# Kernel tuning notes

Hardware: AMD Instinct MI355X
Metric: run time of the kernel (lower is better)

The kernel has to match this reference:

```python
import jax, jax.numpy as jnp
import numpy as np

EPS = 1e-5
ROPE_BASE = 10000.0


def _layernorm(x, g, b):
    mu = jnp.mean(x, axis=-1, keepdims=True)
    var = jnp.mean(jnp.square(x - mu), axis=-1, keepdims=True)
    return (x - mu) * jax.lax.rsqrt(var + EPS) * g + b


def _rope(q, k):
    # q, k: (B, T, H, D); rotate interleaved pairs along last dim, positions over T
    T, D = q.shape[1], q.shape[-1]
    half = D // 2
    inv_freq = ROPE_BASE ** (-jnp.arange(half, dtype=jnp.float32) / half)
    ang = jnp.arange(T, dtype=jnp.float32)[:, None] * inv_freq  # (T, half)
    cos = jnp.cos(ang)[None, :, None, :]
    sin = jnp.sin(ang)[None, :, None, :]

    def rot(x):
        xr, xi = x[..., 0::2], x[..., 1::2]
        yr = xr * cos - xi * sin
        yi = xr * sin + xi * cos
        return jnp.stack([yr, yi], axis=-1).reshape(x.shape)

    return rot(q), rot(k)


def setup_inputs() -> dict:
    key = jax.random.key(0)
    ks = jax.random.split(key, 5)
    E, F, B, T = 1024, 4096, 2, 2048
    s = 0.02
    return {
        "x": jax.random.normal(ks[0], (B, T, E), jnp.float32),
        "in_proj_w": jax.random.normal(ks[1], (3 * E, E), jnp.float32) * s,
        "out_proj_w": jax.random.normal(ks[2], (E, E), jnp.float32) * s,
        "ln1_g": jnp.ones((E,), jnp.float32),
        "ln1_b": jnp.zeros((E,), jnp.float32),
        "ln2_g": jnp.ones((E,), jnp.float32),
        "ln2_b": jnp.zeros((E,), jnp.float32),
        "w1": jax.random.normal(ks[3], (F, E), jnp.float32) * s,
        "w2": jax.random.normal(ks[4], (E, F), jnp.float32) * s,
        "context": 256,
    }


def reference(x, in_proj_w, out_proj_w, ln1_g, ln1_b, ln2_g, ln2_b, w1, w2, context):
    B, T, E = x.shape
    H = 16
    D = E // H

    # ---- self-attention block (pre-norm, residual) ----
    h = _layernorm(x, ln1_g, ln1_b)
    proj = h @ in_proj_w.T  # (B, T, 3E)
    qkv = proj.reshape(B, T, 3, H, D)
    q = qkv[:, :, 0]  # (B, T, H, D)
    k = qkv[:, :, 1]
    v = qkv[:, :, 2].transpose(0, 2, 1, 3)  # (B, H, T, D)
    q, k = _rope(q, k)
    q = q.transpose(0, 2, 1, 3)  # (B, H, T, D)
    k = k.transpose(0, 2, 1, 3)

    pos = jnp.arange(T)
    delta = pos[:, None] - pos[None, :]  # (T, T)
    mask = (delta >= 0) & (delta < context)

    scores = jnp.einsum("bhtd,bhsd->bhts", q, k) / jnp.sqrt(jnp.float32(D))
    scores = jnp.where(mask[None, None], scores, jnp.float32(-1e30))
    attn = jax.nn.softmax(scores, axis=-1)
    o = jnp.einsum("bhts,bhsd->bhtd", attn, v)
    o = o.transpose(0, 2, 1, 3).reshape(B, T, E)
    x = x + o @ out_proj_w.T

    # ---- FFN block (pre-norm, residual) ----
    h = _layernorm(x, ln2_g, ln2_b)
    update = jax.nn.gelu(h @ w1.T, approximate=False) @ w2.T
    return x + update
```

## Files before the change

### kernel.cpp

```cpp
#include <hip/hip_runtime.h>
#include <math.h>

#define B_BATCH 2
#define T_SEQ   2048
#define E_DIM   1024
#define H_HEADS 16
#define D_HEAD  64
#define F_DIM   4096
#define M_ROWS  (B_BATCH * T_SEQ)

typedef __attribute__((ext_vector_type(8))) short short8;
typedef __attribute__((ext_vector_type(4))) float floatx4;
typedef __attribute__((ext_vector_type(8))) unsigned short ushortx8;

typedef __attribute__((address_space(1))) const void global_cvoid;
typedef __attribute__((address_space(3))) void lds_void;

__device__ __forceinline__ unsigned short f2bf(float f) {
    unsigned u = __float_as_uint(f);
    u += 0x7fffu + ((u >> 16) & 1u);
    return (unsigned short)(u >> 16);
}
__device__ __forceinline__ float bf2f(unsigned short h) {
    return __uint_as_float(((unsigned)h) << 16);
}

__device__ __forceinline__ unsigned lds_lo(const void* p) {
    return (unsigned)(unsigned long long)p;
}

__device__ __forceinline__ float gelu_f(float v) {
    const float x = fabsf(v) * 0.70710678118654752f;
    const float t = __builtin_amdgcn_rcpf(__builtin_fmaf(0.3275911f, x, 1.0f));
    float p = __builtin_fmaf(1.061405429f, t, -1.453152027f);
    p = __builtin_fmaf(p, t, 1.421413741f);
    p = __builtin_fmaf(p, t, -0.284496736f);
    p = __builtin_fmaf(p, t, 0.254829592f);
    p *= t;
    const float e = __expf(-x * x);
    float er = __builtin_fmaf(-p, e, 1.0f);
    er = copysignf(er, v);
    return 0.5f * v * (1.0f + er);
}

__device__ __forceinline__ float waveReduceSum(float v) {
#pragma unroll
    for (int off = 32; off > 0; off >>= 1) v += __shfl_xor(v, off, 64);
    return v;
}

__global__ __launch_bounds__(256) void cvt_kernel(const float* __restrict__ in,
                                                  unsigned short* __restrict__ out,
                                                  int n) {
    const int i = (blockIdx.x * 256 + threadIdx.x) * 4;
    if (i >= n) return;
    float4 v = *(const float4*)(in + i);
    ushort4 o;
    o.x = f2bf(v.x); o.y = f2bf(v.y); o.z = f2bf(v.z); o.w = f2bf(v.w);
    *(ushort4*)(out + i) = o;
}

__global__ __launch_bounds__(256) void reduce4_kernel(const float* __restrict__ p,
                                                      float* __restrict__ out, int n) {
    const int i = (blockIdx.x * 256 + threadIdx.x) * 4;
    if (i >= n) return;
    float4 a  = *(const float4*)(out + i);
    float4 b0 = *(const float4*)(p + i);
    float4 b1 = *(const float4*)(p + (size_t)n + i);
    float4 b2 = *(const float4*)(p + 2 * (size_t)n + i);
    float4 b3 = *(const float4*)(p + 3 * (size_t)n + i);
    a.x += b0.x + b1.x + b2.x + b3.x;
    a.y += b0.y + b1.y + b2.y + b3.y;
    a.z += b0.z + b1.z + b2.z + b3.z;
    a.w += b0.w + b1.w + b2.w + b3.w;
    *(float4*)(out + i) = a;
}

__global__ __launch_bounds__(256) void rope_tab_kernel(float* __restrict__ tab) {
    const int idx = blockIdx.x * 256 + threadIdx.x;
    const int pos = idx >> 5, i = idx & 31;
    const float invf = powf(10000.0f, -(float)i / 32.0f);
    const float ang = (float)pos * invf;
    tab[idx * 2]     = cosf(ang);
    tab[idx * 2 + 1] = sinf(ang);
}

__global__ __launch_bounds__(256) void ln_kernel(const float* __restrict__ x,
                                                 const float* __restrict__ g,
                                                 const float* __restrict__ b,
                                                 unsigned short* __restrict__ out) {
    const int row = blockIdx.x;
    const float* xr = x + (size_t)row * E_DIM;
    float4 v = ((const float4*)xr)[threadIdx.x];
    float s  = v.x + v.y + v.z + v.w;
    float sq = v.x * v.x + v.y * v.y + v.z * v.z + v.w * v.w;

    __shared__ float red[8];
    float ws_ = waveReduceSum(s);
    float wq  = waveReduceSum(sq);
    int wid = threadIdx.x >> 6;
    if ((threadIdx.x & 63) == 0) { red[wid] = ws_; red[wid + 4] = wq; }
    __syncthreads();
    float ts = red[0] + red[1] + red[2] + red[3];
    float tq = red[4] + red[5] + red[6] + red[7];
    float mean = ts * (1.0f / E_DIM);
    float var  = tq * (1.0f / E_DIM) - mean * mean;
    float inv  = rsqrtf(var + 1e-5f);

    float4 gv = ((const float4*)g)[threadIdx.x];
    float4 bv = ((const float4*)b)[threadIdx.x];
    ushort4 o;
    o.x = f2bf((v.x - mean) * inv * gv.x + bv.x);
    o.y = f2bf((v.y - mean) * inv * gv.y + bv.y);
    o.z = f2bf((v.z - mean) * inv * gv.z + bv.z);
    o.w = f2bf((v.w - mean) * inv * gv.w + bv.w);
    ((ushort4*)(out + (size_t)row * E_DIM))[threadIdx.x] = o;
}

template <int EPI>
__global__ __launch_bounds__(256) void gemm_bf16(const unsigned short* __restrict__ A,
                                                 const unsigned short* __restrict__ Wt,
                                                 const float* __restrict__ R,
                                                 float* __restrict__ Cf,
                                                 unsigned short* __restrict__ Cb,
                                                 int M, int N, int K) {
    __shared__ unsigned short As[128 * 64];
    __shared__ unsigned short Bs[128 * 64];
    const int tid  = threadIdx.x;
    const int wave = tid >> 6, lane = tid & 63;
    const int wm   = wave >> 1, wn = wave & 1;
    const int quad = lane >> 4, l16 = lane & 15;
    const int m0 = blockIdx.y * 128, n0 = blockIdx.x * 128;
    const int Kc   = K / gridDim.z;
    const int kbeg = blockIdx.z * Kc;

    const int row_rel = lane >> 3;
    const int ch      = lane & 7;

    const floatx4 z = {0.0f, 0.0f, 0.0f, 0.0f};
    floatx4 acc[4][4];
#pragma unroll
    for (int i = 0; i < 4; ++i)
#pragma unroll
        for (int j = 0; j < 4; ++j) acc[i][j] = z;

    for (int k0 = kbeg; k0 < kbeg + Kc; k0 += 64) {
        __syncthreads();
#pragma unroll
        for (int i = 0; i < 4; ++i) {
            const int chunk = wave * 4 + i;
            const int grow  = chunk * 8 + row_rel;
            const int lch   = ch ^ (grow & 7);
            const unsigned short* ga = A  + (size_t)(m0 + grow) * K + k0 + lch * 8;
            const unsigned short* gb = Wt + (size_t)(n0 + grow) * K + k0 + lch * 8;
            __builtin_amdgcn_global_load_lds((global_cvoid*)ga,
                                             (lds_void*)(As + chunk * 512), 16, 0, 0);
            __builtin_amdgcn_global_load_lds((global_cvoid*)gb,
                                             (lds_void*)(Bs + chunk * 512), 16, 0, 0);
        }
        __syncthreads();

#pragma unroll
        for (int ks = 0; ks < 2; ++ks) {
            short8 af[4], bfr[4];
#pragma unroll
            for (int mt = 0; mt < 4; ++mt) {
                const int r = wm * 64 + mt * 16 + l16;
                const int p = (ks * 4 + quad) ^ (r & 7);
                af[mt] = *(const short8*)(As + r * 64 + p * 8);
            }
#pragma unroll
            for (int nt = 0; nt < 4; ++nt) {
                const int r = wn * 64 + nt * 16 + l16;
                const int p = (ks * 4 + quad) ^ (r & 7);
                bfr[nt] = *(const short8*)(Bs + r * 64 + p * 8);
            }
#pragma unroll
            for (int mt = 0; mt < 4; ++mt)
#pragma unroll
                for (int nt = 0; nt < 4; ++nt)
                    acc[mt][nt] = __builtin_amdgcn_mfma_f32_16x16x32_bf16(
                        af[mt], bfr[nt], acc[mt][nt], 0, 0, 0);
        }
    }

#pragma unroll
    for (int mt = 0; mt < 4; ++mt) {
        const int rb = m0 + wm * 64 + mt * 16 + quad * 4;
#pragma unroll
        for (int nt = 0; nt < 4; ++nt) {
            const int col = n0 + wn * 64 + nt * 16 + l16;
#pragma unroll
            for (int r = 0; r < 4; ++r) {
                const size_t idx = (size_t)(rb + r) * N + col;
                const float v = acc[mt][nt][r];
                if (EPI == 1) {
                    Cf[idx] = v + R[idx];
                } else {
                    Cf[idx] = v;
                }
            }
        }
    }
}

template <int EPI>
__global__ __launch_bounds__(512, 2) void gemm256_bf16(const unsigned short* __restrict__ A,
                                                       const unsigned short* __restrict__ Wt,
                                                       float* __restrict__ Cf,
                                                       unsigned short* __restrict__ Cb,
                                                       int M, int N, int K) {
    __shared__ __align__(16) unsigned short Ls[4 * 16384];

    const int tid  = threadIdx.x;
    const int wave = tid >> 6, lane = tid & 63;
    const int wm   = wave >> 2, wn = wave & 3;
    const int quad = lane >> 4, l16 = lane & 15;

    int bid = blockIdx.y * gridDim.x + blockIdx.x;
    const int cpx = (gridDim.x * gridDim.y) >> 3;
    bid = (bid & 7) * cpx + (bid >> 3);
    const int bx = bid % gridDim.x, by = bid / gridDim.x;
    const int m0 = by * 256, n0 = bx * 256;

    const int Kc   = K / gridDim.z;
    const int kbeg = blockIdx.z * Kc;
    const int NT   = Kc >> 5;

    const int rr = lane >> 2;
    const int ch = lane & 3;

    const floatx4 z = {0.0f, 0.0f, 0.0f, 0.0f};
    floatx4 acc[8][4];
#pragma unroll
    for (int i = 0; i < 8; ++i)
#pragma unroll
        for (int j = 0; j < 4; ++j) acc[i][j] = z;

    auto STAGE = [&](int t, int bi) {
        const int k0 = kbeg + t * 32;
#pragma unroll
        for (int i = 0; i < 2; ++i) {
            const int g    = wave * 2 + i;
            const int grow = g * 16 + rr;
            const int sch  = (ch ^ ((grow >> 1) & 3)) * 8;
            const unsigned short* ga = A  + (size_t)(m0 + grow) * K + k0 + sch;
            const unsigned short* gb = Wt + (size_t)(n0 + grow) * K + k0 + sch;
            unsigned short* la = Ls + bi * 16384 + g * 512;
            __builtin_amdgcn_global_load_lds((global_cvoid*)ga, (lds_void*)la,        16, 0, 0);
            __builtin_amdgcn_global_load_lds((global_cvoid*)gb, (lds_void*)(la + 8192), 16, 0, 0);
        }
    };

    const unsigned swz = (unsigned)(quad ^ ((l16 >> 1) & 3));
    const unsigned aA = lds_lo(Ls) + (unsigned)(wm * 128 + l16) * 64u + swz * 16u;
    const unsigned aB = lds_lo(Ls) + 16384u + (unsigned)(wn * 64 + l16) * 64u + swz * 16u;

#define GSTEP(T, C, PD, DOPF, WSTR, DOBAR)                                     \
    do {                                                                       \
        if (DOPF) STAGE((T) + 3, (PD));                                        \
        const unsigned aAc = aA + (C) * 32768u;                                \
        const unsigned aBc = aB + (C) * 32768u;                                \
        short8 af[8], bfr[4];                                                  \
        _Pragma("unroll")                                                      \
        for (int mt = 0; mt < 8; ++mt)                                         \
            asm volatile("ds_read_b128 %0, %1"                                 \
                         : "=v"(af[mt]) : "v"(aAc + mt * 1024u));              \
        _Pragma("unroll")                                                      \
        for (int nt = 0; nt < 4; ++nt)                                         \
            asm volatile("ds_read_b128 %0, %1"                                 \
                         : "=v"(bfr[nt]) : "v"(aBc + nt * 1024u));             \
        asm volatile("s_waitcnt lgkmcnt(0)" ::: "memory");                     \
        __builtin_amdgcn_sched_barrier(0);                                     \
        __builtin_amdgcn_s_setprio(1);                                         \
        _Pragma("unroll")                                                      \
        for (int mt = 0; mt < 8; ++mt)                                         \
            _Pragma("unroll")                                                  \
            for (int nt = 0; nt < 4; ++nt)                                     \
                acc[mt][nt] = __builtin_amdgcn_mfma_f32_16x16x32_bf16(         \
                    af[mt], bfr[nt], acc[mt][nt], 0, 0, 0);                    \
        __builtin_amdgcn_s_setprio(0);                                         \
        if (DOBAR) {                                                           \
            asm volatile("s_waitcnt " WSTR ::: "memory");                      \
            __builtin_amdgcn_s_barrier();                                      \
            __builtin_amdgcn_sched_barrier(0);                                 \
        }                                                                      \
    } while (0)

    STAGE(0, 0);
    STAGE(1, 1);
    STAGE(2, 2);
    asm volatile("s_waitcnt vmcnt(8)" ::: "memory");
    __builtin_amdgcn_s_barrier();
    __builtin_amdgcn_sched_barrier(0);

    int t = 0;
    for (; t + 4 < NT; t += 4) {
        GSTEP(t + 0, 0, 3, true, "vmcnt(8)", true);
        GSTEP(t + 1, 1, 0, true, "vmcnt(8)", true);
        GSTEP(t + 2, 2, 1, true, "vmcnt(8)", true);
        GSTEP(t + 3, 3, 2, true, "vmcnt(8)", true);
    }
    GSTEP(t + 0, 0, 3, true,  "vmcnt(8)", true);
    GSTEP(t + 1, 1, 0, false, "vmcnt(4)", true);
    GSTEP(t + 2, 2, 1, false, "vmcnt(0)", true);
    GSTEP(t + 3, 3, 2, false, "vmcnt(0)", false);
#undef GSTEP

    const size_t zoff = (size_t)blockIdx.z * M * N;
#pragma unroll
    for (int mt = 0; mt < 8; ++mt) {
        const int rb = m0 + wm * 128 + mt * 16 + quad * 4;
#pragma unroll
        for (int nt = 0; nt < 4; ++nt) {
            const int col = n0 + wn * 64 + nt * 16 + l16;
#pragma unroll
            for (int r = 0; r < 4; ++r) {
                const size_t idx = (size_t)(rb + r) * N + col;
                const float v = acc[mt][nt][r];
                if (EPI == 2) {
                    Cb[idx] = f2bf(gelu_f(v));
                } else if (EPI == 4) {
                    Cb[idx] = f2bf(v);
                } else {
                    Cf[zoff + idx] = v;
                }
            }
        }
    }
}

__global__ __launch_bounds__(256) void vtrans_kernel(const unsigned short* __restrict__ proj,
                                                     unsigned short* __restrict__ vt) {
    __shared__ unsigned short L[64 * 72];
    const int bh = blockIdx.y, b = bh >> 4, h = bh & 15;
    const int st = blockIdx.x * 64;
    const int tid = threadIdx.x;
    {
        const int srel = tid >> 2, d16 = (tid & 3) * 16;
        const unsigned short* src =
            proj + (size_t)(b * T_SEQ + st + srel) * (3 * E_DIM) + 2 * E_DIM + h * 64 + d16;
        *(short8*)(L + srel * 72 + d16)     = *(const short8*)(src);
        *(short8*)(L + srel * 72 + d16 + 8) = *(const short8*)(src + 8);
    }
    __syncthreads();
    {
        const int d = tid >> 2, s16 = (tid & 3) * 16;
        short8 o0, o1;
#pragma unroll
        for (int j = 0; j < 8; ++j) {
            o0[j] = (short)L[(s16 + j) * 72 + d];
            o1[j] = (short)L[(s16 + 8 + j) * 72 + d];
        }
        unsigned short* dst = vt + (size_t)(bh * 64 + d) * T_SEQ + st + s16;
        *(short8*)dst       = o0;
        *(short8*)(dst + 8) = o1;
    }
}

__device__ __forceinline__ void rope16(ushortx8 x0, ushortx8 x1, const float* tp,
                                       short8& y0, short8& y1) {
#pragma unroll
    for (int j = 0; j < 4; ++j) {
        const float c = tp[2 * j], s = tp[2 * j + 1];
        const float xr = bf2f(x0[2 * j]), xi = bf2f(x0[2 * j + 1]);
        y0[2 * j]     = (short)f2bf(xr * c - xi * s);
        y0[2 * j + 1] = (short)f2bf(xr * s + xi * c);
    }
#pragma unroll
    for (int j = 0; j < 4; ++j) {
        const float c = tp[8 + 2 * j], s = tp[8 + 2 * j + 1];
        const float xr = bf2f(x1[2 * j]), xi = bf2f(x1[2 * j + 1]);
        y1[2 * j]     = (short)f2bf(xr * c - xi * s);
        y1[2 * j + 1] = (short)f2bf(xr * s + xi * c);
    }
}

__global__ __launch_bounds__(256) void attn_kernel(const unsigned short* __restrict__ proj,
                                                   const unsigned short* __restrict__ vt,
                                                   const float* __restrict__ tab,
                                                   const int* __restrict__ ctxp,
                                                   unsigned short* __restrict__ o) {
    __shared__ unsigned short Qs[64 * 64];
    __shared__ unsigned short Ks[64 * 64];
    __shared__ unsigned short Vs[64 * 64];
    __shared__ unsigned short Ps[4][16 * 64];

    const int ctx = ctxp[0];
    const int tid = threadIdx.x;
    const int wave = tid >> 6, lane = tid & 63;
    const int quad = lane >> 4, l16 = lane & 15;
    const int bh = blockIdx.y, b = bh >> 4, h = bh & 15;
    const int t0 = blockIdx.x * 64;

    {
        const int r = tid >> 2, d16 = (tid & 3) * 16;
        const int pos = t0 + r;
        const unsigned short* src =
            proj + (size_t)(b * T_SEQ + pos) * (3 * E_DIM) + h * 64 + d16;
        ushortx8 x0 = *(const ushortx8*)src;
        ushortx8 x1 = *(const ushortx8*)(src + 8);
        const float* tp = tab + ((size_t)pos * 32 + (d16 >> 1)) * 2;
        short8 y0, y1;
        rope16(x0, x1, tp, y0, y1);
        const int c0 = (tid & 3) * 2;
        *(short8*)(Qs + r * 64 + ((c0)     ^ (r & 7)) * 8) = y0;
        *(short8*)(Qs + r * 64 + ((c0 + 1) ^ (r & 7)) * 8) = y1;
    }

    int first = t0 - (ctx - 1);
    if (first < 0) first = 0;
    const int first_base = first & ~63;

    float m[4] = {-1e30f, -1e30f, -1e30f, -1e30f};
    float l[4] = {0.0f, 0.0f, 0.0f, 0.0f};
    const floatx4 z = {0.0f, 0.0f, 0.0f, 0.0f};
    floatx4 accO[4] = {z, z, z, z};

    const int q_row0 = t0 + wave * 16 + quad * 4;

    for (int s_base = first_base; s_base <= t0; s_base += 64) {
        __syncthreads();
        {
            const int r = tid >> 2, d16 = (tid & 3) * 16;
            const int pos = s_base + r;
            const unsigned short* src =
                proj + (size_t)(b * T_SEQ + pos) * (3 * E_DIM) + E_DIM + h * 64 + d16;
            ushortx8 x0 = *(const ushortx8*)src;
            ushortx8 x1 = *(const ushortx8*)(src + 8);
            const float* tp = tab + ((size_t)pos * 32 + (d16 >> 1)) * 2;
            short8 y0, y1;
            rope16(x0, x1, tp, y0, y1);
            const int c0 = (tid & 3) * 2;
            *(short8*)(Ks + r * 64 + ((c0)     ^ (r & 7)) * 8) = y0;
            *(short8*)(Ks + r * 64 + ((c0 + 1) ^ (r & 7)) * 8) = y1;
        }
#pragma unroll
        for (int i = 0; i < 2; ++i) {
            const int chunk = (wave * 2 + i) * 64 + lane;
            const int d = chunk >> 3, c = chunk & 7;
            const unsigned short* gsrc =
                vt + (size_t)(bh * 64 + d) * T_SEQ + s_base + ((c ^ (d & 7)) * 8);
            __builtin_amdgcn_global_load_lds((global_cvoid*)gsrc,
                                             (lds_void*)(Vs + (wave * 2 + i) * 512),
                                             16, 0, 0);
        }
        __syncthreads();

        floatx4 accS[4] = {z, z, z, z};
#pragma unroll
        for (int ks = 0; ks < 2; ++ks) {
            const int qrow = wave * 16 + l16;
            short8 aq = *(const short8*)(Qs + qrow * 64 + (((ks * 4 + quad) ^ (qrow & 7)) * 8));
#pragma unroll
            for (int nt = 0; nt < 4; ++nt) {
                const int kro = nt * 16 + l16;
                short8 bk = *(const short8*)(Ks + kro * 64 + (((ks * 4 + quad) ^ (kro & 7)) * 8));
                accS[nt] = __builtin_amdgcn_mfma_f32_16x16x32_bf16(aq, bk, accS[nt], 0, 0, 0);
            }
        }

        float p[4][4];
        float alpha[4];
#pragma unroll
        for (int r = 0; r < 4; ++r) {
            const int qa = q_row0 + r;
            float sv[4];
            float vmax = -1e30f;
#pragma unroll
            for (int nt = 0; nt < 4; ++nt) {
                const int sa = s_base + nt * 16 + l16;
                const int dd = qa - sa;
                const bool ok = (unsigned)dd < (unsigned)ctx;
                const float s = ok ? accS[nt][r] * 0.125f : -1e30f;
                sv[nt] = s;
                vmax = fmaxf(vmax, s);
            }
            vmax = fmaxf(vmax, __shfl_xor(vmax, 1));
            vmax = fmaxf(vmax, __shfl_xor(vmax, 2));
            vmax = fmaxf(vmax, __shfl_xor(vmax, 4));
            vmax = fmaxf(vmax, __shfl_xor(vmax, 8));
            const float mn = fmaxf(m[r], vmax);
            alpha[r] = __expf(m[r] - mn);
            float ps = 0.0f;
#pragma unroll
            for (int nt = 0; nt < 4; ++nt) {
                const float pe = (sv[nt] > -0.5e30f) ? __expf(sv[nt] - mn) : 0.0f;
                p[nt][r] = pe;
                ps += pe;
            }
            ps += __shfl_xor(ps, 1);
            ps += __shfl_xor(ps, 2);
            ps += __shfl_xor(ps, 4);
            ps += __shfl_xor(ps, 8);
            l[r] = l[r] * alpha[r] + ps;
            m[r] = mn;
        }

#pragma unroll
        for (int nt = 0; nt < 4; ++nt) {
#pragma unroll
            for (int r = 0; r < 4; ++r) {
                const int row = quad * 4 + r;
                const int col = nt * 16 + l16;
                Ps[wave][row * 64 + (((col >> 3) ^ (row & 7)) * 8) + (col & 7)] =
                    f2bf(p[nt][r]);
            }
        }
#pragma unroll
        for (int nt = 0; nt < 4; ++nt)
#pragma unroll
            for (int r = 0; r < 4; ++r) accO[nt][r] *= alpha[r];

#pragma unroll
        for (int ks = 0; ks < 2; ++ks) {
            short8 ap = *(const short8*)(&Ps[wave][l16 * 64 + (((ks * 4 + quad) ^ (l16 & 7)) * 8)]);
#pragma unroll
            for (int nt = 0; nt < 4; ++nt) {
                const int dr = nt * 16 + l16;
                short8 bv = *(const short8*)(Vs + dr * 64 + (((ks * 4 + quad) ^ (dr & 7)) * 8));
                accO[nt] = __builtin_amdgcn_mfma_f32_16x16x32_bf16(ap, bv, accO[nt], 0, 0, 0);
            }
        }
    }

    float inv[4];
#pragma unroll
    for (int r = 0; r < 4; ++r) inv[r] = 1.0f / l[r];
#pragma unroll
    for (int nt = 0; nt < 4; ++nt) {
#pragma unroll
        for (int r = 0; r < 4; ++r) {
            const int t = q_row0 + r;
            o[(size_t)(b * T_SEQ + t) * E_DIM + h * 64 + nt * 16 + l16] =
                f2bf(accO[nt][r] * inv[r]);
        }
    }
}

extern "C" void kernel_launch(void* const* d_in, const int* in_sizes, int n_in,
                              void* d_out, int out_size, void* d_ws, size_t ws_size,
                              hipStream_t stream) {
    const float* x          = (const float*)d_in[0];
    const float* in_proj_w  = (const float*)d_in[1];
    const float* out_proj_w = (const float*)d_in[2];
    const float* ln1_g      = (const float*)d_in[3];
    const float* ln1_b      = (const float*)d_in[4];
    const float* ln2_g      = (const float*)d_in[5];
    const float* ln2_b      = (const float*)d_in[6];
    const float* w1         = (const float*)d_in[7];
    const float* w2         = (const float*)d_in[8];
    const int*   ctx        = (const int*)d_in[9];
    float* out = (float*)d_out;
    float* ws  = (float*)d_ws;

    const size_t MEG = 1024u * 1024u;
    unsigned short* u = (unsigned short*)ws;
    unsigned short* wqkv_b = u;
    unsigned short* wout_b = u + 3 * MEG;
    unsigned short* w1_b   = u + 4 * MEG;
    unsigned short* h_b    = u + 8 * MEG;
    unsigned short* obuf_b = u + 12 * MEG;
    unsigned short* proj_b = u + 16 * MEG;
    unsigned short* vt_b   = u + 28 * MEG;
    unsigned short* mid_b  = u + 32 * MEG;
    unsigned short* w2_b   = u + 48 * MEG;
    float* tab  = ws + 26 * MEG;
    float* part = ws;

    cvt_kernel<<<3 * E_DIM * E_DIM / 1024, 256, 0, stream>>>(in_proj_w, wqkv_b, 3 * E_DIM * E_DIM);
    cvt_kernel<<<E_DIM * E_DIM / 1024, 256, 0, stream>>>(out_proj_w, wout_b, E_DIM * E_DIM);
    cvt_kernel<<<F_DIM * E_DIM / 1024, 256, 0, stream>>>(w1, w1_b, F_DIM * E_DIM);
    cvt_kernel<<<E_DIM * F_DIM / 1024, 256, 0, stream>>>(w2, w2_b, E_DIM * F_DIM);
    rope_tab_kernel<<<T_SEQ * 32 / 256, 256, 0, stream>>>(tab);

    ln_kernel<<<M_ROWS, 256, 0, stream>>>(x, ln1_g, ln1_b, h_b);
    gemm256_bf16<4><<<dim3(3 * E_DIM / 256, M_ROWS / 256), 512, 0, stream>>>(
        h_b, wqkv_b, nullptr, proj_b, M_ROWS, 3 * E_DIM, E_DIM);
    vtrans_kernel<<<dim3(T_SEQ / 64, B_BATCH * H_HEADS), 256, 0, stream>>>(proj_b, vt_b);
    attn_kernel<<<dim3(T_SEQ / 64, B_BATCH * H_HEADS), 256, 0, stream>>>(
        proj_b, vt_b, tab, ctx, obuf_b);
    gemm_bf16<1><<<dim3(E_DIM / 128, M_ROWS / 128), 256, 0, stream>>>(
        obuf_b, wout_b, x, out, nullptr, M_ROWS, E_DIM, E_DIM);
    ln_kernel<<<M_ROWS, 256, 0, stream>>>(out, ln2_g, ln2_b, h_b);
    gemm256_bf16<2><<<dim3(F_DIM / 256, M_ROWS / 256), 512, 0, stream>>>(
        h_b, w1_b, nullptr, mid_b, M_ROWS, F_DIM, E_DIM);
    gemm256_bf16<5><<<dim3(E_DIM / 256, M_ROWS / 256, 4), 512, 0, stream>>>(
        mid_b, w2_b, part, nullptr, M_ROWS, E_DIM, F_DIM);
    reduce4_kernel<<<M_ROWS * E_DIM / 1024, 256, 0, stream>>>(
        part, out, M_ROWS * E_DIM);
}
```

Before: 325.5 us.

## Fuse prep kernels into one launch and shrink pipelined GEMM tiles to 128x128

Merges the four weight-conversion launches, the RoPE table launch and the first LayerNorm into a single block-indexed prep kernel to cut launch overhead. It also replaces the 256x256, 512-thread pipelined GEMM with a 128x128, 256-thread version for the QKV, FFN1 and FFN2 GEMMs. That gives more blocks for the 256 CUs, at the cost of less operand reuse per block and more global and L2 traffic.

```diff
diff --git a/kernel.cpp b/kernel.cpp
--- a/kernel.cpp
+++ b/kernel.cpp
@@ -49,15 +49,74 @@
     return v;
 }
 
-__global__ __launch_bounds__(256) void cvt_kernel(const float* __restrict__ in,
-                                                  unsigned short* __restrict__ out,
-                                                  int n) {
-    const int i = (blockIdx.x * 256 + threadIdx.x) * 4;
-    if (i >= n) return;
-    float4 v = *(const float4*)(in + i);
+__device__ __forceinline__ void ln_row(const float* __restrict__ x,
+                                       const float* __restrict__ g,
+                                       const float* __restrict__ b,
+                                       unsigned short* __restrict__ out, int row) {
+    const float* xr = x + (size_t)row * E_DIM;
+    float4 v = ((const float4*)xr)[threadIdx.x];
+    float s  = v.x + v.y + v.z + v.w;
+    float sq = v.x * v.x + v.y * v.y + v.z * v.z + v.w * v.w;
+
+    __shared__ float red[8];
+    float ws_ = waveReduceSum(s);
+    float wq  = waveReduceSum(sq);
+    int wid = threadIdx.x >> 6;
+    if ((threadIdx.x & 63) == 0) { red[wid] = ws_; red[wid + 4] = wq; }
+    __syncthreads();
+    float ts = red[0] + red[1] + red[2] + red[3];
+    float tq = red[4] + red[5] + red[6] + red[7];
+    float mean = ts * (1.0f / E_DIM);
+    float var  = tq * (1.0f / E_DIM) - mean * mean;
+    float inv  = rsqrtf(var + 1e-5f);
+
+    float4 gv = ((const float4*)g)[threadIdx.x];
+    float4 bv = ((const float4*)b)[threadIdx.x];
     ushort4 o;
-    o.x = f2bf(v.x); o.y = f2bf(v.y); o.z = f2bf(v.z); o.w = f2bf(v.w);
-    *(ushort4*)(out + i) = o;
+    o.x = f2bf((v.x - mean) * inv * gv.x + bv.x);
+    o.y = f2bf((v.y - mean) * inv * gv.y + bv.y);
+    o.z = f2bf((v.z - mean) * inv * gv.z + bv.z);
+    o.w = f2bf((v.w - mean) * inv * gv.w + bv.w);
+    ((ushort4*)(out + (size_t)row * E_DIM))[threadIdx.x] = o;
+}
+
+__global__ __launch_bounds__(256) void ln_kernel(const float* __restrict__ x,
+                                                 const float* __restrict__ g,
+                                                 const float* __restrict__ b,
+                                                 unsigned short* __restrict__ out) {
+    ln_row(x, g, b, out, blockIdx.x);
+}
+
+__global__ __launch_bounds__(256) void prep_kernel(
+    const float* __restrict__ in_proj_w, const float* __restrict__ out_proj_w,
+    const float* __restrict__ w1, const float* __restrict__ w2,
+    const float* __restrict__ x, const float* __restrict__ ln1_g,
+    const float* __restrict__ ln1_b,
+    unsigned short* __restrict__ wqkv_b, unsigned short* __restrict__ wout_b,
+    unsigned short* __restrict__ w1_b, unsigned short* __restrict__ w2_b,
+    unsigned short* __restrict__ h_b, float* __restrict__ tab) {
+    const int blk = blockIdx.x;
+    if (blk < 12288) {
+        const float* src; unsigned short* dst; int base;
+        if (blk < 3072)      { src = in_proj_w;  dst = wqkv_b; base = blk; }
+        else if (blk < 4096) { src = out_proj_w; dst = wout_b; base = blk - 3072; }
+        else if (blk < 8192) { src = w1;         dst = w1_b;   base = blk - 4096; }
+        else                 { src = w2;         dst = w2_b;   base = blk - 8192; }
+        const int i = (base * 256 + threadIdx.x) * 4;
+        float4 v = *(const float4*)(src + i);
+        ushort4 o;
+        o.x = f2bf(v.x); o.y = f2bf(v.y); o.z = f2bf(v.z); o.w = f2bf(v.w);
+        *(ushort4*)(dst + i) = o;
+    } else if (blk < 12544) {
+        const int idx = (blk - 12288) * 256 + threadIdx.x;
+        const int pos = idx >> 5, i = idx & 31;
+        const float invf = powf(10000.0f, -(float)i / 32.0f);
+        const float ang = (float)pos * invf;
+        tab[idx * 2]     = cosf(ang);
+        tab[idx * 2 + 1] = sinf(ang);
+    } else {
+        ln_row(x, ln1_g, ln1_b, h_b, blk - 12544);
+    }
 }
 
 __global__ __launch_bounds__(256) void reduce4_kernel(const float* __restrict__ p,
@@ -74,47 +133,6 @@
     a.z += b0.z + b1.z + b2.z + b3.z;
     a.w += b0.w + b1.w + b2.w + b3.w;
     *(float4*)(out + i) = a;
-}
-
-__global__ __launch_bounds__(256) void rope_tab_kernel(float* __restrict__ tab) {
-    const int idx = blockIdx.x * 256 + threadIdx.x;
-    const int pos = idx >> 5, i = idx & 31;
-    const float invf = powf(10000.0f, -(float)i / 32.0f);
-    const float ang = (float)pos * invf;
-    tab[idx * 2]     = cosf(ang);
-    tab[idx * 2 + 1] = sinf(ang);
-}
-
-__global__ __launch_bounds__(256) void ln_kernel(const float* __restrict__ x,
-                                                 const float* __restrict__ g,
-                                                 const float* __restrict__ b,
-                                                 unsigned short* __restrict__ out) {
-    const int row = blockIdx.x;
-    const float* xr = x + (size_t)row * E_DIM;
-    float4 v = ((const float4*)xr)[threadIdx.x];
-    float s  = v.x + v.y + v.z + v.w;
-    float sq = v.x * v.x + v.y * v.y + v.z * v.z + v.w * v.w;
-
-    __shared__ float red[8];
-    float ws_ = waveReduceSum(s);
-    float wq  = waveReduceSum(sq);
-    int wid = threadIdx.x >> 6;
-    if ((threadIdx.x & 63) == 0) { red[wid] = ws_; red[wid + 4] = wq; }
-    __syncthreads();
-    float ts = red[0] + red[1] + red[2] + red[3];
-    float tq = red[4] + red[5] + red[6] + red[7];
-    float mean = ts * (1.0f / E_DIM);
-    float var  = tq * (1.0f / E_DIM) - mean * mean;
-    float inv  = rsqrtf(var + 1e-5f);
-
-    float4 gv = ((const float4*)g)[threadIdx.x];
-    float4 bv = ((const float4*)b)[threadIdx.x];
-    ushort4 o;
-    o.x = f2bf((v.x - mean) * inv * gv.x + bv.x);
-    o.y = f2bf((v.y - mean) * inv * gv.y + bv.y);
-    o.z = f2bf((v.z - mean) * inv * gv.z + bv.z);
-    o.w = f2bf((v.w - mean) * inv * gv.w + bv.w);
-    ((ushort4*)(out + (size_t)row * E_DIM))[threadIdx.x] = o;
 }
 
 template <int EPI>
@@ -205,35 +223,35 @@
 }
 
 template <int EPI>
-__global__ __launch_bounds__(512, 2) void gemm256_bf16(const unsigned short* __restrict__ A,
-                                                       const unsigned short* __restrict__ Wt,
-                                                       float* __restrict__ Cf,
-                                                       unsigned short* __restrict__ Cb,
-                                                       int M, int N, int K) {
-    __shared__ __align__(16) unsigned short Ls[4 * 16384];
+__global__ __launch_bounds__(256, 2) void gemm128p_bf16(const unsigned short* __restrict__ A,
+                                                        const unsigned short* __restrict__ Wt,
+                                                        float* __restrict__ Cf,
+                                                        unsigned short* __restrict__ Cb,
+                                                        int M, int N, int K) {
+    __shared__ __align__(16) unsigned short Ls[4 * 8192];
 
     const int tid  = threadIdx.x;
     const int wave = tid >> 6, lane = tid & 63;
-    const int wm   = wave >> 2, wn = wave & 3;
+    const int wm   = wave >> 1, wn = wave & 1;
     const int quad = lane >> 4, l16 = lane & 15;
 
     int bid = blockIdx.y * gridDim.x + blockIdx.x;
     const int cpx = (gridDim.x * gridDim.y) >> 3;
     bid = (bid & 7) * cpx + (bid >> 3);
     const int bx = bid % gridDim.x, by = bid / gridDim.x;
-    const int m0 = by * 256, n0 = bx * 256;
+    const int m0 = by * 128, n0 = bx * 128;
 
     const int Kc   = K / gridDim.z;
     const int kbeg = blockIdx.z * Kc;
     const int NT   = Kc >> 5;
 
-    const int rr = lane >> 2;
-    const int ch = lane & 3;
+    const int rr4 = lane >> 2;
+    const int ch4 = lane & 3;
 
     const floatx4 z = {0.0f, 0.0f, 0.0f, 0.0f};
-    floatx4 acc[8][4];
-#pragma unroll
-    for (int i = 0; i < 8; ++i)
+    floatx4 acc[4][4];
+#pragma unroll
+    for (int i = 0; i < 4; ++i)
 #pragma unroll
         for (int j = 0; j < 4; ++j) acc[i][j] = z;
 
@@ -242,28 +260,28 @@
 #pragma unroll
         for (int i = 0; i < 2; ++i) {
             const int g    = wave * 2 + i;
-            const int grow = g * 16 + rr;
-            const int sch  = (ch ^ ((grow >> 1) & 3)) * 8;
+            const int grow = g * 16 + rr4;
+            const int sch  = (ch4 ^ ((grow >> 1) & 3)) * 8;
             const unsigned short* ga = A  + (size_t)(m0 + grow) * K + k0 + sch;
             const unsigned short* gb = Wt + (size_t)(n0 + grow) * K + k0 + sch;
-            unsigned short* la = Ls + bi * 16384 + g * 512;
+            unsigned short* la = Ls + bi * 8192 + g * 512;
             __builtin_amdgcn_global_load_lds((global_cvoid*)ga, (lds_void*)la,        16, 0, 0);
-            __builtin_amdgcn_global_load_lds((global_cvoid*)gb, (lds_void*)(la + 8192), 16, 0, 0);
+            __builtin_amdgcn_global_load_lds((global_cvoid*)gb, (lds_void*)(la + 4096), 16, 0, 0);
         }
     };
 
     const unsigned swz = (unsigned)(quad ^ ((l16 >> 1) & 3));
-    const unsigned aA = lds_lo(Ls) + (unsigned)(wm * 128 + l16) * 64u + swz * 16u;
-    const unsigned aB = lds_lo(Ls) + 16384u + (unsigned)(wn * 64 + l16) * 64u + swz * 16u;
+    const unsigned aA = lds_lo(Ls) + (unsigned)(wm * 64 + l16) * 64u + swz * 16u;
+    const unsigned aB = lds_lo(Ls) + 8192u + (unsigned)(wn * 64 + l16) * 64u + swz * 16u;
 
 #define GSTEP(T, C, PD, DOPF, WSTR, DOBAR)                                     \
     do {                                                                       \
         if (DOPF) STAGE((T) + 3, (PD));                                        \
-        const unsigned aAc = aA + (C) * 32768u;                                \
-        const unsigned aBc = aB + (C) * 32768u;                                \
-        short8 af[8], bfr[4];                                                  \
+        const unsigned aAc = aA + (C) * 16384u;                                \
+        const unsigned aBc = aB + (C) * 16384u;                                \
+        short8 af[4], bfr[4];                                                  \
         _Pragma("unroll")                                                      \
-        for (int mt = 0; mt < 8; ++mt)                                         \
+        for (int mt = 0; mt < 4; ++mt)                                         \
             asm volatile("ds_read_b128 %0, %1"                                 \
                          : "=v"(af[mt]) : "v"(aAc + mt * 1024u));              \
         _Pragma("unroll")                                                      \
@@ -274,7 +292,7 @@
         __builtin_amdgcn_sched_barrier(0);                                     \
         __builtin_amdgcn_s_setprio(1);                                         \
         _Pragma("unroll")                                                      \
-        for (int mt = 0; mt < 8; ++mt)                                         \
+        for (int mt = 0; mt < 4; ++mt)                                         \
             _Pragma("unroll")                                                  \
             for (int nt = 0; nt < 4; ++nt)                                     \
                 acc[mt][nt] = __builtin_amdgcn_mfma_f32_16x16x32_bf16(         \
@@ -309,8 +327,8 @@
 
     const size_t zoff = (size_t)blockIdx.z * M * N;
 #pragma unroll
-    for (int mt = 0; mt < 8; ++mt) {
-        const int rb = m0 + wm * 128 + mt * 16 + quad * 4;
+    for (int mt = 0; mt < 4; ++mt) {
+        const int rb = m0 + wm * 64 + mt * 16 + quad * 4;
 #pragma unroll
         for (int nt = 0; nt < 4; ++nt) {
             const int col = n0 + wn * 64 + nt * 16 + l16;
@@ -568,14 +586,10 @@
     float* tab  = ws + 26 * MEG;
     float* part = ws;
 
-    cvt_kernel<<<3 * E_DIM * E_DIM / 1024, 256, 0, stream>>>(in_proj_w, wqkv_b, 3 * E_DIM * E_DIM);
-    cvt_kernel<<<E_DIM * E_DIM / 1024, 256, 0, stream>>>(out_proj_w, wout_b, E_DIM * E_DIM);
-    cvt_kernel<<<F_DIM * E_DIM / 1024, 256, 0, stream>>>(w1, w1_b, F_DIM * E_DIM);
-    cvt_kernel<<<E_DIM * F_DIM / 1024, 256, 0, stream>>>(w2, w2_b, E_DIM * F_DIM);
-    rope_tab_kernel<<<T_SEQ * 32 / 256, 256, 0, stream>>>(tab);
-
-    ln_kernel<<<M_ROWS, 256, 0, stream>>>(x, ln1_g, ln1_b, h_b);
-    gemm256_bf16<4><<<dim3(3 * E_DIM / 256, M_ROWS / 256), 512, 0, stream>>>(
+    prep_kernel<<<16640, 256, 0, stream>>>(in_proj_w, out_proj_w, w1, w2,
+                                           x, ln1_g, ln1_b,
+                                           wqkv_b, wout_b, w1_b, w2_b, h_b, tab);
+    gemm128p_bf16<4><<<dim3(3 * E_DIM / 128, M_ROWS / 128), 256, 0, stream>>>(
         h_b, wqkv_b, nullptr, proj_b, M_ROWS, 3 * E_DIM, E_DIM);
     vtrans_kernel<<<dim3(T_SEQ / 64, B_BATCH * H_HEADS), 256, 0, stream>>>(proj_b, vt_b);
     attn_kernel<<<dim3(T_SEQ / 64, B_BATCH * H_HEADS), 256, 0, stream>>>(
@@ -583,9 +597,9 @@
     gemm_bf16<1><<<dim3(E_DIM / 128, M_ROWS / 128), 256, 0, stream>>>(
         obuf_b, wout_b, x, out, nullptr, M_ROWS, E_DIM, E_DIM);
     ln_kernel<<<M_ROWS, 256, 0, stream>>>(out, ln2_g, ln2_b, h_b);
-    gemm256_bf16<2><<<dim3(F_DIM / 256, M_ROWS / 256), 512, 0, stream>>>(
+    gemm128p_bf16<2><<<dim3(F_DIM / 128, M_ROWS / 128), 256, 0, stream>>>(
         h_b, w1_b, nullptr, mid_b, M_ROWS, F_DIM, E_DIM);
-    gemm256_bf16<5><<<dim3(E_DIM / 256, M_ROWS / 256, 4), 512, 0, stream>>>(
+    gemm128p_bf16<5><<<dim3(E_DIM / 128, M_ROWS / 128, 4), 256, 0, stream>>>(
         mid_b, w2_b, part, nullptr, M_ROWS, E_DIM, F_DIM);
     reduce4_kernel<<<M_ROWS * E_DIM / 1024, 256, 0, stream>>>(
         part, out, M_ROWS * E_DIM);
```

Result: no change. 319.5 us (-1.9%).
